# Kernel tuning notes

Hardware: AMD Instinct MI355X
Metric: run time of the kernel (lower is better)

## Reference

```python
import jax, jax.numpy as jnp
import numpy as np

B, N, D = 32, 64, 256
PENALTY = 10000.0
TEMP = 0.05
N_ITERS = 20


def setup_inputs() -> dict:
    key = jax.random.key(0)
    ks = jax.random.split(key, 8)
    f32 = jnp.float32
    return {
        "slots_t": jax.random.normal(ks[0], (B, N, D), f32),
        "slots_t1": jax.random.normal(ks[1], (B, N, D), f32),
        "alive_t": jax.random.uniform(ks[2], (B, N), f32),
        "alive_t1": jax.random.uniform(ks[3], (B, N), f32),
        "W1": jax.random.normal(ks[4], (3 * D, D), f32) / np.float32(np.sqrt(3 * D)),
        "b1": jnp.zeros((D,), f32),
        "W2": jax.random.normal(ks[5], (D, D // 4), f32) / np.float32(np.sqrt(D)),
        "b2": jnp.zeros((D // 4,), f32),
        "W3": jax.random.normal(ks[6], (D // 4, 1), f32) / np.float32(np.sqrt(D // 4)),
        "b3": jnp.zeros((1,), f32),
    }


def reference(slots_t, slots_t1, alive_t, alive_t1, W1, b1, W2, b2, W3, b3):
    # ---- cost matrix: pairwise expand + tiny MLP ----
    s_t = jnp.clip(slots_t, -50.0, 50.0)    # (B,N,D)
    s_t1 = jnp.clip(slots_t1, -50.0, 50.0)  # (B,N,D)
    s_t_exp = jnp.broadcast_to(s_t[:, :, None, :], (B, N, N, D))
    s_t1_exp = jnp.broadcast_to(s_t1[:, None, :, :], (B, N, N, D))
    diff = jnp.abs(s_t_exp - s_t1_exp)
    pair_feat = jnp.concatenate([s_t_exp, s_t1_exp, diff], axis=-1)  # (B,N,N,3D)
    h = jax.nn.relu(pair_feat @ W1 + b1)       # (B,N,N,D)
    h = jax.nn.relu(h @ W2 + b2)               # (B,N,N,D/4)
    score = (h @ W3 + b3)[..., 0]              # (B,N,N)
    dead_t = (alive_t < 0.5).astype(score.dtype)
    dead_t1 = (alive_t1 < 0.5).astype(score.dtype)
    score = score - PENALTY * dead_t[:, :, None] - PENALTY * dead_t1[:, None, :]
    cost = jnp.clip(-score, -PENALTY, PENALTY)
    # ---- Sinkhorn (log-space) ----
    log_alpha = -cost / TEMP

    def step(la, _):
        la = la - jax.nn.logsumexp(la, axis=2, keepdims=True)
        la = la - jax.nn.logsumexp(la, axis=1, keepdims=True)
        return la, None

    log_alpha, _ = jax.lax.scan(step, log_alpha, None, length=N_ITERS)
    assignment = jnp.exp(log_alpha)            # (B,N,N)
    perm = jnp.argmax(assignment, axis=2)      # (B,N)
    confidence = jnp.max(assignment, axis=2)   # (B,N)
    # ---- matched mask ----
    alive_t_hard = (alive_t > 0.5).astype(assignment.dtype)
    alive_t1_hard = (alive_t1 > 0.5).astype(assignment.dtype)
    matched_t1 = jnp.take_along_axis(alive_t1_hard, perm, axis=1)
    matched = alive_t_hard * matched_t1 * (confidence > 0.3).astype(assignment.dtype)
    return perm, matched
```

## Files before the change

kernel.cpp:

```cpp
#include <hip/hip_runtime.h>

#define NB 32
#define NN 64
#define ND 256
#define MH 32
constexpr float PEN = 10000.0f;
constexpr float TEMP_ = 0.05f;

typedef __bf16 bfrag __attribute__((ext_vector_type(8)));
typedef float  f32x4 __attribute__((ext_vector_type(4)));

__device__ __forceinline__ float clip50(float x) { return fminf(fmaxf(x, -50.0f), 50.0f); }

__device__ __forceinline__ ushort bf16_rne(float x) {
    uint u = __builtin_bit_cast(uint, x);
    return (ushort)((u + 0x7fffu + ((u >> 16) & 1u)) >> 16);
}
__device__ __forceinline__ void split2(float a, float b, uint& h, uint& l) {
    const ushort ha = bf16_rne(a), hb = bf16_rne(b);
    const float fa = __builtin_bit_cast(float, (uint)ha << 16);
    const float fb = __builtin_bit_cast(float, (uint)hb << 16);
    const ushort la = bf16_rne(a - fa), lb = bf16_rne(b - fb);
    h = (uint)ha | ((uint)hb << 16);
    l = (uint)la | ((uint)lb << 16);
}
#define ASW(m, k2) ((m) * 512 + ((k2) ^ (((m) & 7) << 4)))

__global__ __launch_bounds__(256)
void k01_uv_pack(const float* __restrict__ s_t, const float* __restrict__ s_t1,
                 const float* __restrict__ W1, const float* __restrict__ b1,
                 const float* __restrict__ W2, float* __restrict__ U,
                 float* __restrict__ V, ushort* __restrict__ w1h,
                 ushort* __restrict__ w1l, ushort* __restrict__ w2h,
                 ushort* __restrict__ w2l)
{
    const int tid = threadIdx.x;
    if (blockIdx.x >= 512) {
        const int gid = (blockIdx.x - 512) * 256 + tid;
        const float* srcW; ushort *dh, *dl;
        int fb, kt, col, kbase, stride, base;
        if (gid < 8192) {
            fb = gid >> 6; kt = fb >> 4;
            const int ntg = fb & 15, ln = gid & 63;
            col = ntg * 16 + (ln & 15); kbase = kt * 32 + (ln >> 4) * 8;
            srcW = W1 + 2 * ND * ND; stride = ND; dh = w1h; dl = w1l; base = gid * 8;
        } else {
            const int g2 = gid - 8192;
            fb = g2 >> 6; kt = fb >> 2;
            const int ntg = fb & 3, ln = g2 & 63;
            col = ntg * 16 + (ln & 15); kbase = kt * 32 + (ln >> 4) * 8;
            srcW = W2; stride = 64; dh = w2h; dl = w2l; base = g2 * 8;
        }
        uint hv[4], lv[4];
        #pragma unroll
        for (int p = 0; p < 4; ++p) {
            const float a = srcW[(kbase + 2 * p) * stride + col];
            const float b = srcW[(kbase + 2 * p + 1) * stride + col];
            split2(a, b, hv[p], lv[p]);
        }
        *(uint4*)(dh + base) = make_uint4(hv[0], hv[1], hv[2], hv[3]);
        *(uint4*)(dl + base) = make_uint4(lv[0], lv[1], lv[2], lv[3]);
        return;
    }
    const int half = blockIdx.x >> 8;
    const int rem  = blockIdx.x & 255;
    const int rb   = rem >> 1;
    const int colh = rem & 1;
    const float* src = half ? s_t1 : s_t;
    const float* W   = W1 + half * ND * ND;
    float* dst = half ? V : U;
    __shared__ float sL[16 * ND];
    const int rbase = rb * 16;
    #pragma unroll
    for (int t = 0; t < 4; ++t) {
        const int i4 = ((t << 8) + tid) << 2;
        float4 a = *(const float4*)(src + rbase * ND + i4);
        a.x = clip50(a.x); a.y = clip50(a.y); a.z = clip50(a.z); a.w = clip50(a.w);
        *(float4*)(sL + i4) = a;
    }
    __syncthreads();
    const int wv   = tid >> 6;
    const int lane = tid & 63;
    const int tj1  = lane >> 5;
    const int tc   = lane & 31;
    const int r0   = wv * 4 + tj1 * 2;
    const int c0   = colh * 128 + tc * 4;
    float acc[2][4] = {};
    for (int k4 = 0; k4 < ND; k4 += 4) {
        float4 sv[2];
        #pragma unroll
        for (int r = 0; r < 2; ++r) sv[r] = *(const float4*)(sL + (r0 + r) * ND + k4);
        #pragma unroll
        for (int kk = 0; kk < 4; ++kk) {
            const float4 wvv = *(const float4*)(W + (k4 + kk) * ND + c0);
            #pragma unroll
            for (int r = 0; r < 2; ++r) {
                const float s = (&sv[r].x)[kk];
                acc[r][0] = fmaf(s, wvv.x, acc[r][0]);
                acc[r][1] = fmaf(s, wvv.y, acc[r][1]);
                acc[r][2] = fmaf(s, wvv.z, acc[r][2]);
                acc[r][3] = fmaf(s, wvv.w, acc[r][3]);
            }
        }
    }
    float4 bias = make_float4(0.f, 0.f, 0.f, 0.f);
    if (!half) bias = *(const float4*)(b1 + c0);
    #pragma unroll
    for (int r = 0; r < 2; ++r) {
        float4 o;
        o.x = acc[r][0] + bias.x; o.y = acc[r][1] + bias.y;
        o.z = acc[r][2] + bias.z; o.w = acc[r][3] + bias.w;
        *(float4*)(dst + (rbase + r0 + r) * ND + c0) = o;
    }
}

__global__ __launch_bounds__(256, 4)
void k2_scores(const float* __restrict__ s_t, const float* __restrict__ s_t1,
               const float* __restrict__ b2, const float* __restrict__ W3,
               const float* __restrict__ b3, const float* __restrict__ alive_t,
               const float* __restrict__ alive_t1,
               const float* __restrict__ U, const float* __restrict__ V,
               const ushort* __restrict__ w1h, const ushort* __restrict__ w1l,
               const ushort* __restrict__ w2h, const ushort* __restrict__ w2l,
               float* __restrict__ laG)
{
    __shared__ ushort sAh[MH * ND];
    __shared__ ushort sAl[MH * ND];
    __shared__ float  red[4 * MH];
    const int tid = threadIdx.x;
    const int bi  = blockIdx.x >> 1;
    const int jh  = blockIdx.x & 1;
    const int b   = bi >> 6;
    const int jbase = jh * MH;
    const int lane = tid & 63;
    const int w    = tid >> 6;
    const int mlane = lane & 15;
    const int kg    = lane >> 4;

    {
        const float* stb = s_t + bi * ND;
        const float* s1b = s_t1 + (size_t)b * NN * ND + (size_t)jbase * ND;
        #pragma unroll
        for (int t = 0; t < 4; ++t) {
            const int slot = (t << 8) + tid;
            const int m  = slot >> 5;
            const int k0 = (slot & 31) << 3;
            const float4 a0 = *(const float4*)(stb + k0);
            const float4 a1 = *(const float4*)(stb + k0 + 4);
            const float4 p0 = *(const float4*)(s1b + m * ND + k0);
            const float4 p1 = *(const float4*)(s1b + m * ND + k0 + 4);
            float d[8];
            d[0] = fabsf(clip50(a0.x) - clip50(p0.x));
            d[1] = fabsf(clip50(a0.y) - clip50(p0.y));
            d[2] = fabsf(clip50(a0.z) - clip50(p0.z));
            d[3] = fabsf(clip50(a0.w) - clip50(p0.w));
            d[4] = fabsf(clip50(a1.x) - clip50(p1.x));
            d[5] = fabsf(clip50(a1.y) - clip50(p1.y));
            d[6] = fabsf(clip50(a1.z) - clip50(p1.z));
            d[7] = fabsf(clip50(a1.w) - clip50(p1.w));
            uint hv[4], lv[4];
            #pragma unroll
            for (int p = 0; p < 4; ++p) split2(d[2*p], d[2*p+1], hv[p], lv[p]);
            const int off = ASW(m, k0 * 2);
            *(uint4*)((char*)sAh + off) = make_uint4(hv[0], hv[1], hv[2], hv[3]);
            *(uint4*)((char*)sAl + off) = make_uint4(lv[0], lv[1], lv[2], lv[3]);
        }
    }
    __syncthreads();

    f32x4 acc[2][4];
    #pragma unroll
    for (int mt = 0; mt < 2; ++mt)
        #pragma unroll
        for (int nt = 0; nt < 4; ++nt)
            #pragma unroll
            for (int r = 0; r < 4; ++r) acc[mt][nt][r] = 0.f;
    #pragma unroll
    for (int kt = 0; kt < 8; ++kt) {
        bfrag Bh[4], Bl[4], Ah[2], Al[2];
        #pragma unroll
        for (int nt = 0; nt < 4; ++nt) {
            const int fo = (kt * 16 + (w << 2) + nt) * 512 + lane * 8;
            Bh[nt] = *(const bfrag*)(w1h + fo);
            Bl[nt] = *(const bfrag*)(w1l + fo);
        }
        const int k2b = (kt * 32 + kg * 8) * 2;
        #pragma unroll
        for (int mt = 0; mt < 2; ++mt) {
            const int m = mt * 16 + mlane;
            const int off = ASW(m, k2b);
            Ah[mt] = *(const bfrag*)((const char*)sAh + off);
            Al[mt] = *(const bfrag*)((const char*)sAl + off);
        }
        #pragma unroll
        for (int mt = 0; mt < 2; ++mt)
            #pragma unroll
            for (int nt = 0; nt < 4; ++nt) {
                acc[mt][nt] = __builtin_amdgcn_mfma_f32_16x16x32_bf16(Ah[mt], Bh[nt], acc[mt][nt], 0, 0, 0);
                acc[mt][nt] = __builtin_amdgcn_mfma_f32_16x16x32_bf16(Ah[mt], Bl[nt], acc[mt][nt], 0, 0, 0);
                acc[mt][nt] = __builtin_amdgcn_mfma_f32_16x16x32_bf16(Al[mt], Bh[nt], acc[mt][nt], 0, 0, 0);
            }
    }
    __syncthreads();

    {
        const float* Ur = U + (size_t)bi * ND;
        const float* Vb = V + (size_t)b * NN * ND + (size_t)jbase * ND;
        float Uc[4];
        #pragma unroll
        for (int nt = 0; nt < 4; ++nt) Uc[nt] = Ur[w * 64 + nt * 16 + mlane];
        #pragma unroll
        for (int mt = 0; mt < 2; ++mt) {
            #pragma unroll
            for (int r = 0; r < 4; ++r) {
                const int j = mt * 16 + (kg << 2) + r;
                const float* Vr = Vb + (size_t)j * ND;
                #pragma unroll
                for (int nt = 0; nt < 4; ++nt) {
                    const int c = w * 64 + nt * 16 + mlane;
                    float x = acc[mt][nt][r] + Uc[nt] + Vr[c];
                    x = fmaxf(x, 0.f);
                    const ushort hh = bf16_rne(x);
                    const float  fh = __builtin_bit_cast(float, (uint)hh << 16);
                    const ushort ll = bf16_rne(x - fh);
                    const int off = ASW(j, c * 2);
                    *(ushort*)((char*)sAh + off) = hh;
                    *(ushort*)((char*)sAl + off) = ll;
                }
            }
        }
    }
    __syncthreads();

    f32x4 acc2[2];
    #pragma unroll
    for (int mt = 0; mt < 2; ++mt)
        #pragma unroll
        for (int r = 0; r < 4; ++r) acc2[mt][r] = 0.f;
    #pragma unroll
    for (int kt = 0; kt < 8; ++kt) {
        const int fo = (kt * 4 + w) * 512 + lane * 8;
        const bfrag Bh = *(const bfrag*)(w2h + fo);
        const bfrag Bl = *(const bfrag*)(w2l + fo);
        const int k2b = (kt * 32 + kg * 8) * 2;
        #pragma unroll
        for (int mt = 0; mt < 2; ++mt) {
            const int m = mt * 16 + mlane;
            const int off = ASW(m, k2b);
            const bfrag Ah = *(const bfrag*)((const char*)sAh + off);
            const bfrag Al = *(const bfrag*)((const char*)sAl + off);
            acc2[mt] = __builtin_amdgcn_mfma_f32_16x16x32_bf16(Ah, Bh, acc2[mt], 0, 0, 0);
            acc2[mt] = __builtin_amdgcn_mfma_f32_16x16x32_bf16(Ah, Bl, acc2[mt], 0, 0, 0);
            acc2[mt] = __builtin_amdgcn_mfma_f32_16x16x32_bf16(Al, Bh, acc2[mt], 0, 0, 0);
        }
    }

    {
        const int m = w * 16 + mlane;
        const float b2v = b2[m];
        const float w3v = W3[m];
        #pragma unroll
        for (int mt = 0; mt < 2; ++mt) {
            #pragma unroll
            for (int r = 0; r < 4; ++r) {
                const int j = mt * 16 + (kg << 2) + r;
                float val = fmaxf(acc2[mt][r] + b2v, 0.f) * w3v;
                val += __shfl_xor(val, 1, 64);
                val += __shfl_xor(val, 2, 64);
                val += __shfl_xor(val, 4, 64);
                val += __shfl_xor(val, 8, 64);
                if (mlane == 0) red[w * MH + j] = val;
            }
        }
    }
    __syncthreads();
    if (tid < MH) {
        const int j = tid;
        const float sc = red[j] + red[MH + j] + red[2 * MH + j] + red[3 * MH + j] + b3[0];
        const float pen_i = (alive_t[bi] < 0.5f) ? PEN : 0.0f;
        const float pj = (alive_t1[b * NN + jbase + j] < 0.5f) ? PEN : 0.0f;
        const float sp = sc - pen_i - pj;
        laG[bi * NN + jbase + j] = fminf(fmaxf(sp, -PEN), PEN) / TEMP_;
    }
}

__global__ __launch_bounds__(256)
void k3_sinkhorn(const float* __restrict__ laG, const float* __restrict__ alive_t,
                 const float* __restrict__ alive_t1, float* __restrict__ out)
{
    __shared__ float la[NN * 65];
    const int b = blockIdx.x, tid = threadIdx.x;
    for (int idx = tid; idx < NN * NN; idx += 256)
        la[(idx >> 6) * 65 + (idx & 63)] = laG[b * NN * NN + idx];
    __syncthreads();

    const int g = tid >> 2;
    const int q = tid & 3;
    for (int it = 0; it < 20; ++it) {
        {
            float m = -INFINITY;
            #pragma unroll
            for (int t = 0; t < 16; ++t) m = fmaxf(m, la[g * 65 + q * 16 + t]);
            m = fmaxf(m, __shfl_xor(m, 1, 64));
            m = fmaxf(m, __shfl_xor(m, 2, 64));
            float s = 0.f;
            #pragma unroll
            for (int t = 0; t < 16; ++t) s += expf(la[g * 65 + q * 16 + t] - m);
            s += __shfl_xor(s, 1, 64);
            s += __shfl_xor(s, 2, 64);
            const float lse = m + logf(s);
            #pragma unroll
            for (int t = 0; t < 16; ++t) la[g * 65 + q * 16 + t] -= lse;
        }
        __syncthreads();
        {
            float m = -INFINITY;
            #pragma unroll
            for (int t = 0; t < 16; ++t) m = fmaxf(m, la[(q * 16 + t) * 65 + g]);
            m = fmaxf(m, __shfl_xor(m, 1, 64));
            m = fmaxf(m, __shfl_xor(m, 2, 64));
            float s = 0.f;
            #pragma unroll
            for (int t = 0; t < 16; ++t) s += expf(la[(q * 16 + t) * 65 + g] - m);
            s += __shfl_xor(s, 1, 64);
            s += __shfl_xor(s, 2, 64);
            const float lse = m + logf(s);
            #pragma unroll
            for (int t = 0; t < 16; ++t) la[(q * 16 + t) * 65 + g] -= lse;
        }
        __syncthreads();
    }

    float bm = -INFINITY; int bidx = 0;
    #pragma unroll
    for (int t = 0; t < 16; ++t) {
        const float v = la[g * 65 + q * 16 + t];
        if (v > bm) { bm = v; bidx = q * 16 + t; }
    }
    #pragma unroll
    for (int off = 1; off < 4; off <<= 1) {
        const float om = __shfl_xor(bm, off, 64);
        const int   oi = __shfl_xor(bidx, off, 64);
        if (om > bm || (om == bm && oi < bidx)) { bm = om; bidx = oi; }
    }
    if (q == 0) {
        const float conf = expf(bm);
        const float at  = alive_t[b * NN + g];
        const float at1 = alive_t1[b * NN + bidx];
        const float matched = (at > 0.5f && at1 > 0.5f && conf > 0.3f) ? 1.0f : 0.0f;
        out[b * NN + g] = (float)bidx;
        out[NB * NN + b * NN + g] = matched;
    }
}

extern "C" void kernel_launch(void* const* d_in, const int* in_sizes, int n_in,
                              void* d_out, int out_size, void* d_ws, size_t ws_size,
                              hipStream_t stream)
{
    (void)in_sizes; (void)n_in; (void)out_size; (void)ws_size;
    const float* s_t      = (const float*)d_in[0];
    const float* s_t1     = (const float*)d_in[1];
    const float* alive_t  = (const float*)d_in[2];
    const float* alive_t1 = (const float*)d_in[3];
    const float* W1 = (const float*)d_in[4];
    const float* b1 = (const float*)d_in[5];
    const float* W2 = (const float*)d_in[6];
    const float* b2 = (const float*)d_in[7];
    const float* W3 = (const float*)d_in[8];
    const float* b3 = (const float*)d_in[9];

    char* ws = (char*)d_ws;
    float*  U   = (float*)(ws);
    float*  V   = (float*)(ws + 2097152);
    float*  laG = (float*)(ws + 4194304);
    ushort* w1h = (ushort*)(ws + 4718592);
    ushort* w1l = (ushort*)(ws + 4849664);
    ushort* w2h = (ushort*)(ws + 4980736);
    ushort* w2l = (ushort*)(ws + 5013504);
    float* out = (float*)d_out;

    hipLaunchKernelGGL(k01_uv_pack, dim3(552), dim3(256), 0, stream,
                       s_t, s_t1, W1, b1, W2, U, V, w1h, w1l, w2h, w2l);
    hipLaunchKernelGGL(k2_scores, dim3(NB * NN * 2), dim3(256), 0, stream,
                       s_t, s_t1, b2, W3, b3, alive_t, alive_t1, U, V,
                       w1h, w1l, w2h, w2l, laG);
    hipLaunchKernelGGL(k3_sinkhorn, dim3(NB), dim3(256), 0, stream,
                       laG, alive_t, alive_t1, out);
}
```

Measured before the change: 207.7 us.

## Swap MFMA operand roles, vectorize epilogue stores, widen Sinkhorn block to 512

The first GEMM in the score kernel now passes the W1 fragments as the A operand and the activations as B. Each lane's accumulator then holds four consecutive output columns, so the epilogue can use float4 loads of U and V and packed uint2 stores to LDS instead of scalar loads and 16-bit stores. The bf16 hi/lo split uses native __bf16 conversions instead of manual bit rounding. The Sinkhorn kernel runs 512 threads with 8 lanes per row, which halves the serial work per thread but adds a shuffle stage per reduction.

```diff
diff --git a/kernel.cpp b/kernel.cpp
--- a/kernel.cpp
+++ b/kernel.cpp
@@ -11,7 +11,10 @@
 typedef float  f32x4 __attribute__((ext_vector_type(4)));
 
 __device__ __forceinline__ float clip50(float x) { return fminf(fmaxf(x, -50.0f), 50.0f); }
-
+__device__ __forceinline__ ushort bfbits(__bf16 h) { return __builtin_bit_cast(ushort, h); }
+__device__ __forceinline__ float bf2f(__bf16 h) {
+    return __builtin_bit_cast(float, (uint)bfbits(h) << 16);
+}
 __device__ __forceinline__ ushort bf16_rne(float x) {
     uint u = __builtin_bit_cast(uint, x);
     return (ushort)((u + 0x7fffu + ((u >> 16) & 1u)) >> 16);
@@ -160,7 +163,13 @@
             d[7] = fabsf(clip50(a1.w) - clip50(p1.w));
             uint hv[4], lv[4];
             #pragma unroll
-            for (int p = 0; p < 4; ++p) split2(d[2*p], d[2*p+1], hv[p], lv[p]);
+            for (int p = 0; p < 4; ++p) {
+                const __bf16 ha = (__bf16)d[2*p], hb = (__bf16)d[2*p+1];
+                const __bf16 la_ = (__bf16)(d[2*p]   - bf2f(ha));
+                const __bf16 lb_ = (__bf16)(d[2*p+1] - bf2f(hb));
+                hv[p] = (uint)bfbits(ha) | ((uint)bfbits(hb) << 16);
+                lv[p] = (uint)bfbits(la_) | ((uint)bfbits(lb_) << 16);
+            }
             const int off = ASW(m, k0 * 2);
             *(uint4*)((char*)sAh + off) = make_uint4(hv[0], hv[1], hv[2], hv[3]);
             *(uint4*)((char*)sAl + off) = make_uint4(lv[0], lv[1], lv[2], lv[3]);
@@ -168,37 +177,36 @@
     }
     __syncthreads();
 
-    f32x4 acc[2][4];
-    #pragma unroll
-    for (int mt = 0; mt < 2; ++mt)
-        #pragma unroll
-        for (int nt = 0; nt < 4; ++nt)
-            #pragma unroll
-            for (int r = 0; r < 4; ++r) acc[mt][nt][r] = 0.f;
+    f32x4 acc[4][2];
+    #pragma unroll
+    for (int ct = 0; ct < 4; ++ct)
+        #pragma unroll
+        for (int jt = 0; jt < 2; ++jt)
+            #pragma unroll
+            for (int r = 0; r < 4; ++r) acc[ct][jt][r] = 0.f;
     #pragma unroll
     for (int kt = 0; kt < 8; ++kt) {
-        bfrag Bh[4], Bl[4], Ah[2], Al[2];
-        #pragma unroll
-        for (int nt = 0; nt < 4; ++nt) {
-            const int fo = (kt * 16 + (w << 2) + nt) * 512 + lane * 8;
-            Bh[nt] = *(const bfrag*)(w1h + fo);
-            Bl[nt] = *(const bfrag*)(w1l + fo);
+        bfrag Ah[4], Al[4], Bh[2], Bl[2];
+        #pragma unroll
+        for (int ct = 0; ct < 4; ++ct) {
+            const int fo = (kt * 16 + (w << 2) + ct) * 512 + lane * 8;
+            Ah[ct] = *(const bfrag*)(w1h + fo);
+            Al[ct] = *(const bfrag*)(w1l + fo);
         }
         const int k2b = (kt * 32 + kg * 8) * 2;
         #pragma unroll
-        for (int mt = 0; mt < 2; ++mt) {
-            const int m = mt * 16 + mlane;
-            const int off = ASW(m, k2b);
-            Ah[mt] = *(const bfrag*)((const char*)sAh + off);
-            Al[mt] = *(const bfrag*)((const char*)sAl + off);
-        }
-        #pragma unroll
-        for (int mt = 0; mt < 2; ++mt)
-            #pragma unroll
-            for (int nt = 0; nt < 4; ++nt) {
-                acc[mt][nt] = __builtin_amdgcn_mfma_f32_16x16x32_bf16(Ah[mt], Bh[nt], acc[mt][nt], 0, 0, 0);
-                acc[mt][nt] = __builtin_amdgcn_mfma_f32_16x16x32_bf16(Ah[mt], Bl[nt], acc[mt][nt], 0, 0, 0);
-                acc[mt][nt] = __builtin_amdgcn_mfma_f32_16x16x32_bf16(Al[mt], Bh[nt], acc[mt][nt], 0, 0, 0);
+        for (int jt = 0; jt < 2; ++jt) {
+            const int off = ASW(jt * 16 + mlane, k2b);
+            Bh[jt] = *(const bfrag*)((const char*)sAh + off);
+            Bl[jt] = *(const bfrag*)((const char*)sAl + off);
+        }
+        #pragma unroll
+        for (int ct = 0; ct < 4; ++ct)
+            #pragma unroll
+            for (int jt = 0; jt < 2; ++jt) {
+                acc[ct][jt] = __builtin_amdgcn_mfma_f32_16x16x32_bf16(Ah[ct], Bh[jt], acc[ct][jt], 0, 0, 0);
+                acc[ct][jt] = __builtin_amdgcn_mfma_f32_16x16x32_bf16(Ah[ct], Bl[jt], acc[ct][jt], 0, 0, 0);
+                acc[ct][jt] = __builtin_amdgcn_mfma_f32_16x16x32_bf16(Al[ct], Bh[jt], acc[ct][jt], 0, 0, 0);
             }
     }
     __syncthreads();
@@ -206,27 +214,31 @@
     {
         const float* Ur = U + (size_t)bi * ND;
         const float* Vb = V + (size_t)b * NN * ND + (size_t)jbase * ND;
-        float Uc[4];
-        #pragma unroll
-        for (int nt = 0; nt < 4; ++nt) Uc[nt] = Ur[w * 64 + nt * 16 + mlane];
-        #pragma unroll
-        for (int mt = 0; mt < 2; ++mt) {
-            #pragma unroll
-            for (int r = 0; r < 4; ++r) {
-                const int j = mt * 16 + (kg << 2) + r;
-                const float* Vr = Vb + (size_t)j * ND;
-                #pragma unroll
-                for (int nt = 0; nt < 4; ++nt) {
-                    const int c = w * 64 + nt * 16 + mlane;
-                    float x = acc[mt][nt][r] + Uc[nt] + Vr[c];
-                    x = fmaxf(x, 0.f);
-                    const ushort hh = bf16_rne(x);
-                    const float  fh = __builtin_bit_cast(float, (uint)hh << 16);
-                    const ushort ll = bf16_rne(x - fh);
-                    const int off = ASW(j, c * 2);
-                    *(ushort*)((char*)sAh + off) = hh;
-                    *(ushort*)((char*)sAl + off) = ll;
-                }
+        #pragma unroll
+        for (int ct = 0; ct < 4; ++ct) {
+            const int c0 = (w << 6) + ct * 16 + (kg << 2);
+            const float4 uq = *(const float4*)(Ur + c0);
+            #pragma unroll
+            for (int jt = 0; jt < 2; ++jt) {
+                const int j = jt * 16 + mlane;
+                const float4 vq = *(const float4*)(Vb + (size_t)j * ND + c0);
+                float x[4];
+                x[0] = fmaxf(acc[ct][jt][0] + uq.x + vq.x, 0.f);
+                x[1] = fmaxf(acc[ct][jt][1] + uq.y + vq.y, 0.f);
+                x[2] = fmaxf(acc[ct][jt][2] + uq.z + vq.z, 0.f);
+                x[3] = fmaxf(acc[ct][jt][3] + uq.w + vq.w, 0.f);
+                const __bf16 h0 = (__bf16)x[0], h1v = (__bf16)x[1];
+                const __bf16 h2 = (__bf16)x[2], h3 = (__bf16)x[3];
+                const __bf16 l0 = (__bf16)(x[0] - bf2f(h0)), l1 = (__bf16)(x[1] - bf2f(h1v));
+                const __bf16 l2 = (__bf16)(x[2] - bf2f(h2)), l3 = (__bf16)(x[3] - bf2f(h3));
+                uint2 hq, lq;
+                hq.x = (uint)bfbits(h0) | ((uint)bfbits(h1v) << 16);
+                hq.y = (uint)bfbits(h2) | ((uint)bfbits(h3) << 16);
+                lq.x = (uint)bfbits(l0) | ((uint)bfbits(l1) << 16);
+                lq.y = (uint)bfbits(l2) | ((uint)bfbits(l3) << 16);
+                const int off = ASW(j, c0 * 2);
+                *(uint2*)((char*)sAh + off) = hq;
+                *(uint2*)((char*)sAl + off) = lq;
             }
         }
     }
@@ -284,61 +296,65 @@
     }
 }
 
-__global__ __launch_bounds__(256)
+__global__ __launch_bounds__(512)
 void k3_sinkhorn(const float* __restrict__ laG, const float* __restrict__ alive_t,
                  const float* __restrict__ alive_t1, float* __restrict__ out)
 {
     __shared__ float la[NN * 65];
     const int b = blockIdx.x, tid = threadIdx.x;
-    for (int idx = tid; idx < NN * NN; idx += 256)
+    for (int idx = tid; idx < NN * NN; idx += 512)
         la[(idx >> 6) * 65 + (idx & 63)] = laG[b * NN * NN + idx];
     __syncthreads();
 
-    const int g = tid >> 2;
-    const int q = tid & 3;
+    const int g = tid >> 3;
+    const int q = tid & 7;
     for (int it = 0; it < 20; ++it) {
         {
             float m = -INFINITY;
             #pragma unroll
-            for (int t = 0; t < 16; ++t) m = fmaxf(m, la[g * 65 + q * 16 + t]);
+            for (int t = 0; t < 8; ++t) m = fmaxf(m, la[g * 65 + q * 8 + t]);
             m = fmaxf(m, __shfl_xor(m, 1, 64));
             m = fmaxf(m, __shfl_xor(m, 2, 64));
+            m = fmaxf(m, __shfl_xor(m, 4, 64));
             float s = 0.f;
             #pragma unroll
-            for (int t = 0; t < 16; ++t) s += expf(la[g * 65 + q * 16 + t] - m);
+            for (int t = 0; t < 8; ++t) s += expf(la[g * 65 + q * 8 + t] - m);
             s += __shfl_xor(s, 1, 64);
             s += __shfl_xor(s, 2, 64);
+            s += __shfl_xor(s, 4, 64);
             const float lse = m + logf(s);
             #pragma unroll
-            for (int t = 0; t < 16; ++t) la[g * 65 + q * 16 + t] -= lse;
+            for (int t = 0; t < 8; ++t) la[g * 65 + q * 8 + t] -= lse;
         }
         __syncthreads();
         {
             float m = -INFINITY;
             #pragma unroll
-            for (int t = 0; t < 16; ++t) m = fmaxf(m, la[(q * 16 + t) * 65 + g]);
+            for (int t = 0; t < 8; ++t) m = fmaxf(m, la[(q * 8 + t) * 65 + g]);
             m = fmaxf(m, __shfl_xor(m, 1, 64));
             m = fmaxf(m, __shfl_xor(m, 2, 64));
+            m = fmaxf(m, __shfl_xor(m, 4, 64));
             float s = 0.f;
             #pragma unroll
-            for (int t = 0; t < 16; ++t) s += expf(la[(q * 16 + t) * 65 + g] - m);
+            for (int t = 0; t < 8; ++t) s += expf(la[(q * 8 + t) * 65 + g] - m);
             s += __shfl_xor(s, 1, 64);
             s += __shfl_xor(s, 2, 64);
+            s += __shfl_xor(s, 4, 64);
             const float lse = m + logf(s);
             #pragma unroll
-            for (int t = 0; t < 16; ++t) la[(q * 16 + t) * 65 + g] -= lse;
+            for (int t = 0; t < 8; ++t) la[(q * 8 + t) * 65 + g] -= lse;
         }
         __syncthreads();
     }
 
     float bm = -INFINITY; int bidx = 0;
     #pragma unroll
-    for (int t = 0; t < 16; ++t) {
-        const float v = la[g * 65 + q * 16 + t];
-        if (v > bm) { bm = v; bidx = q * 16 + t; }
-    }
-    #pragma unroll
-    for (int off = 1; off < 4; off <<= 1) {
+    for (int t = 0; t < 8; ++t) {
+        const float v = la[g * 65 + q * 8 + t];
+        if (v > bm) { bm = v; bidx = q * 8 + t; }
+    }
+    #pragma unroll
+    for (int off = 1; off < 8; off <<= 1) {
         const float om = __shfl_xor(bm, off, 64);
         const int   oi = __shfl_xor(bidx, off, 64);
         if (om > bm || (om == bm && oi < bidx)) { bm = om; bidx = oi; }
@@ -384,6 +400,6 @@
     hipLaunchKernelGGL(k2_scores, dim3(NB * NN * 2), dim3(256), 0, stream,
                        s_t, s_t1, b2, W3, b3, alive_t, alive_t1, U, V,
                        w1h, w1l, w2h, w2l, laG);
-    hipLaunchKernelGGL(k3_sinkhorn, dim3(NB), dim3(256), 0, stream,
+    hipLaunchKernelGGL(k3_sinkhorn, dim3(NB), dim3(512), 0, stream,
                        laG, alive_t, alive_t1, out);
 }
```

Result: faster. 201.3 us (-3.1%).
